# Performance work log

Hardware: AMD Instinct MI355X
Metric: run time of the kernel (lower is better)

Reference implementation:

```python
import jax, jax.numpy as jnp
import numpy as np

NUM_NODES = 100000
NUM_EDGES = 1600000
IN_DIM = 128
NUM_HEADS = 4
HEAD_DIM = 32  # out_dim=128, concat=True
NEG_SLOPE = 0.2
EPS = 1e-16


def setup_inputs() -> dict:
    key = jax.random.key(0)
    k1, k2, k3, k4 = jax.random.split(key, 4)
    node_features = jax.random.normal(k1, (NUM_NODES, IN_DIM), dtype=jnp.float32)
    edge_index = jax.random.randint(k2, (2, NUM_EDGES), 0, NUM_NODES, dtype=jnp.int64)
    W = jax.random.normal(k3, (IN_DIM, NUM_HEADS * HEAD_DIM), dtype=jnp.float32) * 0.05
    a = jax.random.normal(k4, (NUM_HEADS, 2 * HEAD_DIM), dtype=jnp.float32)
    return {"node_features": node_features, "edge_index": edge_index, "W": W, "a": a}


def reference(node_features, edge_index, W, a):
    N = node_features.shape[0]
    # h: [N, H, hd]
    h = (node_features @ W).reshape(N, NUM_HEADS, HEAD_DIM)
    src, dst = edge_index[0], edge_index[1]
    h_src = h[src]  # [E, H, hd]
    h_dst = h[dst]  # [E, H, hd]
    # a . cat(h_src, h_dst) split into two dots to avoid materializing h_cat
    scores = (jnp.einsum('ehd,hd->eh', h_src, a[:, :HEAD_DIM])
              + jnp.einsum('ehd,hd->eh', h_dst, a[:, HEAD_DIM:]))
    scores = jnp.where(scores >= 0, scores, NEG_SLOPE * scores)  # leaky_relu(0.2)
    # scatter-softmax over incoming edges of each dst node (unstabilized exp, as in source)
    exp_s = jnp.exp(scores)  # [E, H]
    sum_exp = jax.ops.segment_sum(exp_s, dst, num_segments=N)  # [N, H]
    attn = exp_s / (sum_exp[dst] + EPS)  # [E, H]
    # dropout is identity in eval mode
    weighted = h_src * attn[:, :, None]  # [E, H, hd]
    out = jax.ops.segment_sum(weighted.reshape(-1, NUM_HEADS * HEAD_DIM), dst, num_segments=N)
    return out  # [N, out_dim]
```

## Files before the change

kernel.cpp:

```cpp
#include <hip/hip_runtime.h>

#define NN 100000
#define NE 1600000

#define NRANGE 256
#define RDST 391
#define CAP 6800
#define EPB_A 16384
#define NCHA ((NE + EPB_A - 1) / EPB_A)
#define GEMM_BLK 1563

typedef __attribute__((ext_vector_type(8))) __bf16 bf16x8;
typedef __attribute__((ext_vector_type(4))) float  f32x4;

static __device__ __forceinline__ unsigned f2bf(float f) {
    unsigned u = __float_as_uint(f);
    return (u + 0x7fffu + ((u >> 16) & 1u)) >> 16;
}
static __device__ __forceinline__ float bf2f(unsigned b) {
    return __uint_as_float(b << 16);
}

union PkA { unsigned u[4]; bf16x8 b; };

__global__ __launch_bounds__(256) void kA_prep_bin(
    const float* __restrict__ W, const float* __restrict__ a,
    uint4* __restrict__ B0g, uint4* __restrict__ B1g,
    const int* __restrict__ ei, int* __restrict__ rangeRes,
    unsigned* __restrict__ bins)
{
    __shared__ float sWa[1024];
    __shared__ int cnt[NRANGE], base[NRANGE], cur[NRANGE];
    const int t = threadIdx.x;

    if (blockIdx.x == 0) {
        for (int e = t; e < 1024; e += 256) {
            int k = e >> 3, j = e & 7, q = j >> 1, s = j & 1;
            float sum = 0.f;
            #pragma unroll
            for (int c = 0; c < 32; ++c)
                sum = fmaf(W[k * 128 + q * 32 + c], a[q * 64 + s * 32 + c], sum);
            sWa[e] = sum;
        }
        __syncthreads();
        #pragma unroll
        for (int it = 0; it < 9; ++it) {
            int f  = it * 256 + t;
            int l  = f & 63;
            int tk = (f >> 6) & 3;
            int tn = f >> 8;
            int col = tn * 16 + (l & 15);
            int kk  = tk * 32 + ((l >> 4) << 3);
            unsigned hb[8], lb[8];
            #pragma unroll
            for (int j = 0; j < 8; ++j) {
                float w;
                if (col < 128)       w = W[(kk + j) * 128 + col];
                else if (col < 136)  w = sWa[(kk + j) * 8 + (col - 128)];
                else                 w = 0.f;
                hb[j] = f2bf(w);
                lb[j] = f2bf(w - bf2f(hb[j]));
            }
            B0g[f] = make_uint4(hb[0] | (hb[1] << 16), hb[2] | (hb[3] << 16),
                                hb[4] | (hb[5] << 16), hb[6] | (hb[7] << 16));
            B1g[f] = make_uint4(lb[0] | (lb[1] << 16), lb[2] | (lb[3] << 16),
                                lb[4] | (lb[5] << 16), lb[6] | (lb[7] << 16));
        }
        return;
    }

    const int c  = blockIdx.x - 1;
    const int b0 = c * EPB_A;
    const int b1 = min(NE, b0 + EPB_A);

    cnt[t] = 0;
    __syncthreads();
    for (int i = b0 + t; i < b1; i += 256)
        atomicAdd(&cnt[ei[NE + i] / RDST], 1);
    __syncthreads();
    base[t] = atomicAdd(&rangeRes[t * 16], cnt[t]) + t * CAP;
    cur[t] = 0;
    __syncthreads();
    for (int i = b0 + t; i < b1; i += 256) {
        int s = ei[i], d = ei[NE + i];
        int r = d / RDST;
        unsigned dloc = (unsigned)(d - r * RDST);
        int off = atomicAdd(&cur[r], 1);
        bins[base[r] + off] = (dloc << 17) | (unsigned)s;
    }
}

__global__ __launch_bounds__(256) void kB_gemm_build(
    const float* __restrict__ X, const uint4* __restrict__ B0g,
    const uint4* __restrict__ B1g, unsigned short* __restrict__ h16,
    float* __restrict__ asrc, float* __restrict__ adst,
    const int* __restrict__ rangeRes, const unsigned* __restrict__ bins,
    int* __restrict__ csr_src, int* __restrict__ cursor)
{
    __shared__ unsigned short B0[9 * 4 * 64 * 8];
    __shared__ unsigned short B1[9 * 4 * 64 * 8];
    const int tid = threadIdx.x;

    if (blockIdx.x < GEMM_BLK) {
        {
            uint4* s0 = (uint4*)B0;
            uint4* s1 = (uint4*)B1;
            #pragma unroll
            for (int it = 0; it < 9; ++it) {
                s0[it * 256 + tid] = B0g[it * 256 + tid];
                s1[it * 256 + tid] = B1g[it * 256 + tid];
            }
        }
        __syncthreads();

        const int w = tid >> 6;
        const int l = tid & 63;
        const int rowbase = blockIdx.x * 64 + w * 16;
        const int row = rowbase + (l & 15);
        const int rowc = row < NN ? row : (NN - 1);
        const float* xr = X + (size_t)rowc * 128 + ((l >> 4) << 3);

        f32x4 acc[9];
        #pragma unroll
        for (int t = 0; t < 9; ++t) acc[t] = (f32x4){0.f, 0.f, 0.f, 0.f};

        #pragma unroll
        for (int tk = 0; tk < 4; ++tk) {
            float4 xa = *(const float4*)(xr + tk * 32);
            float4 xb = *(const float4*)(xr + tk * 32 + 4);
            PkA pa;
            pa.u[0] = f2bf(xa.x) | (f2bf(xa.y) << 16);
            pa.u[1] = f2bf(xa.z) | (f2bf(xa.w) << 16);
            pa.u[2] = f2bf(xb.x) | (f2bf(xb.y) << 16);
            pa.u[3] = f2bf(xb.z) | (f2bf(xb.w) << 16);
            #pragma unroll
            for (int tn = 0; tn < 9; ++tn) {
                int off = (((tn << 2) + tk) * 64 + l) * 8;
                bf16x8 bh = *reinterpret_cast<const bf16x8*>(&B0[off]);
                bf16x8 bl = *reinterpret_cast<const bf16x8*>(&B1[off]);
                acc[tn] = __builtin_amdgcn_mfma_f32_16x16x32_bf16(pa.b, bh, acc[tn], 0, 0, 0);
                acc[tn] = __builtin_amdgcn_mfma_f32_16x16x32_bf16(pa.b, bl, acc[tn], 0, 0, 0);
            }
        }

        __syncthreads();

        const int g = l >> 4;
        unsigned short* hs = B0 + w * 2048;
        #pragma unroll
        for (int tn = 0; tn < 8; ++tn) {
            #pragma unroll
            for (int r = 0; r < 4; ++r)
                hs[((g << 2) + r) * 128 + (tn << 4) + (l & 15)] =
                    (unsigned short)f2bf(acc[tn][r]);
        }
        if ((l & 15) < 8) {
            int j = l & 15, q = j >> 1, s = j & 1;
            float* dp = s ? adst : asrc;
            #pragma unroll
            for (int r = 0; r < 4; ++r) {
                int rr = rowbase + (g << 2) + r;
                if (rr < NN) dp[rr * 4 + q] = acc[8][r];
            }
        }
        __syncthreads();

        if (rowbase < NN) {
            const uint4* sp = (const uint4*)hs;
            uint4* dp = (uint4*)(h16 + (size_t)rowbase * 128);
            #pragma unroll
            for (int i = 0; i < 4; ++i) dp[i * 64 + l] = sp[i * 64 + l];
        }
        return;
    }

    int* lenS = (int*)B0;
    int* hist = lenS + NRANGE;
    int* cur  = hist + 512;
    const int r = blockIdx.x - GEMM_BLK;
    const int t = tid;

    lenS[t] = rangeRes[t * 16];
    __syncthreads();
    for (int off = 1; off < NRANGE; off <<= 1) {
        int v = (t >= off) ? lenS[t - off] : 0;
        __syncthreads();
        lenS[t] += v;
        __syncthreads();
    }
    const int rangeOff = r ? lenS[r - 1] : 0;
    const int n = lenS[r] - rangeOff;
    const int lo = r * RDST;
    const int nd = min(RDST, NN - lo);

    hist[t] = 0; hist[t + 256] = 0;
    __syncthreads();
    const unsigned* bp = bins + (size_t)r * CAP;
    for (int i = t; i < n; i += 256)
        atomicAdd(&hist[bp[i] >> 17], 1);
    __syncthreads();
    for (int off = 1; off < 512; off <<= 1) {
        int i0 = t, i1 = t + 256;
        int v0 = (i0 >= off) ? hist[i0 - off] : 0;
        int v1 = (i1 >= off) ? hist[i1 - off] : 0;
        __syncthreads();
        hist[i0] += v0; hist[i1] += v1;
        __syncthreads();
    }
    for (int b = t; b < RDST; b += 256) cur[b] = b ? hist[b - 1] : 0;
    __syncthreads();
    for (int i = t; i < n; i += 256) {
        unsigned v = bp[i];
        int pos = atomicAdd(&cur[v >> 17], 1);
        csr_src[rangeOff + pos] = (int)(v & 0x1FFFFu);
    }
    __syncthreads();
    for (int b = t; b < nd; b += 256) cursor[lo + b] = rangeOff + cur[b];
}

__global__ __launch_bounds__(256) void k4_agg(
    const int* __restrict__ cursor, const int* __restrict__ csr_src,
    const float* __restrict__ asrc, const float* __restrict__ adst,
    const unsigned short* __restrict__ h16, float* __restrict__ out)
{
    int wid = (blockIdx.x * 256 + threadIdx.x) >> 6;
    if (wid >= NN) return;
    int l = threadIdx.x & 63;
    int g = l >> 4;
    int cidx = l & 15;
    int head = cidx >> 2;

    int end = cursor[wid];
    int beg = wid ? cursor[wid - 1] : 0;

    float ad = adst[(size_t)wid * 4 + head];

    float acc[8];
    #pragma unroll
    for (int c = 0; c < 8; ++c) acc[c] = 0.f;
    float sum = 0.f;

    int i = beg + g;
    if (i < end) {
        const int last = end - 1;
        int s0 = csr_src[i];
        int s1 = csr_src[min(i + 4,  last)];
        int s2 = csr_src[min(i + 8,  last)];
        int s3 = csr_src[min(i + 12, last)];
        do {
            int i2 = i + 16;
            int t0 = csr_src[min(i2,      last)];
            int t1 = csr_src[min(i2 + 4,  last)];
            int t2 = csr_src[min(i2 + 8,  last)];
            int t3 = csr_src[min(i2 + 12, last)];

            float a0 = asrc[(size_t)s0 * 4 + head];
            uint4 h0 = *(const uint4*)(h16 + (size_t)s0 * 128 + cidx * 8);
            float a1 = asrc[(size_t)s1 * 4 + head];
            uint4 h1 = *(const uint4*)(h16 + (size_t)s1 * 128 + cidx * 8);
            float a2 = asrc[(size_t)s2 * 4 + head];
            uint4 h2 = *(const uint4*)(h16 + (size_t)s2 * 128 + cidx * 8);
            float a3 = asrc[(size_t)s3 * 4 + head];
            uint4 h3 = *(const uint4*)(h16 + (size_t)s3 * 128 + cidx * 8);

            float sc0 = a0 + ad; sc0 = sc0 >= 0.f ? sc0 : 0.2f * sc0;
            float sc1 = a1 + ad; sc1 = sc1 >= 0.f ? sc1 : 0.2f * sc1;
            float sc2 = a2 + ad; sc2 = sc2 >= 0.f ? sc2 : 0.2f * sc2;
            float sc3 = a3 + ad; sc3 = sc3 >= 0.f ? sc3 : 0.2f * sc3;
            float w0 = __expf(sc0);
            float w1 = (i + 4  <= last) ? __expf(sc1) : 0.f;
            float w2 = (i + 8  <= last) ? __expf(sc2) : 0.f;
            float w3 = (i + 12 <= last) ? __expf(sc3) : 0.f;
            sum += (w0 + w1) + (w2 + w3);

            acc[0] = fmaf(w0, __uint_as_float(h0.x << 16),         acc[0]);
            acc[1] = fmaf(w0, __uint_as_float(h0.x & 0xffff0000u), acc[1]);
            acc[2] = fmaf(w0, __uint_as_float(h0.y << 16),         acc[2]);
            acc[3] = fmaf(w0, __uint_as_float(h0.y & 0xffff0000u), acc[3]);
            acc[4] = fmaf(w0, __uint_as_float(h0.z << 16),         acc[4]);
            acc[5] = fmaf(w0, __uint_as_float(h0.z & 0xffff0000u), acc[5]);
            acc[6] = fmaf(w0, __uint_as_float(h0.w << 16),         acc[6]);
            acc[7] = fmaf(w0, __uint_as_float(h0.w & 0xffff0000u), acc[7]);

            acc[0] = fmaf(w1, __uint_as_float(h1.x << 16),         acc[0]);
            acc[1] = fmaf(w1, __uint_as_float(h1.x & 0xffff0000u), acc[1]);
            acc[2] = fmaf(w1, __uint_as_float(h1.y << 16),         acc[2]);
            acc[3] = fmaf(w1, __uint_as_float(h1.y & 0xffff0000u), acc[3]);
            acc[4] = fmaf(w1, __uint_as_float(h1.z << 16),         acc[4]);
            acc[5] = fmaf(w1, __uint_as_float(h1.z & 0xffff0000u), acc[5]);
            acc[6] = fmaf(w1, __uint_as_float(h1.w << 16),         acc[6]);
            acc[7] = fmaf(w1, __uint_as_float(h1.w & 0xffff0000u), acc[7]);

            acc[0] = fmaf(w2, __uint_as_float(h2.x << 16),         acc[0]);
            acc[1] = fmaf(w2, __uint_as_float(h2.x & 0xffff0000u), acc[1]);
            acc[2] = fmaf(w2, __uint_as_float(h2.y << 16),         acc[2]);
            acc[3] = fmaf(w2, __uint_as_float(h2.y & 0xffff0000u), acc[3]);
            acc[4] = fmaf(w2, __uint_as_float(h2.z << 16),         acc[4]);
            acc[5] = fmaf(w2, __uint_as_float(h2.z & 0xffff0000u), acc[5]);
            acc[6] = fmaf(w2, __uint_as_float(h2.w << 16),         acc[6]);
            acc[7] = fmaf(w2, __uint_as_float(h2.w & 0xffff0000u), acc[7]);

            acc[0] = fmaf(w3, __uint_as_float(h3.x << 16),         acc[0]);
            acc[1] = fmaf(w3, __uint_as_float(h3.x & 0xffff0000u), acc[1]);
            acc[2] = fmaf(w3, __uint_as_float(h3.y << 16),         acc[2]);
            acc[3] = fmaf(w3, __uint_as_float(h3.y & 0xffff0000u), acc[3]);
            acc[4] = fmaf(w3, __uint_as_float(h3.z << 16),         acc[4]);
            acc[5] = fmaf(w3, __uint_as_float(h3.z & 0xffff0000u), acc[5]);
            acc[6] = fmaf(w3, __uint_as_float(h3.w << 16),         acc[6]);
            acc[7] = fmaf(w3, __uint_as_float(h3.w & 0xffff0000u), acc[7]);

            s0 = t0; s1 = t1; s2 = t2; s3 = t3; i = i2;
        } while (i < end);
    }

    #pragma unroll
    for (int c = 0; c < 8; ++c) {
        acc[c] += __shfl_xor(acc[c], 16);
        acc[c] += __shfl_xor(acc[c], 32);
    }
    sum += __shfl_xor(sum, 16);
    sum += __shfl_xor(sum, 32);

    if (g == 0) {
        float rs = 1.0f / (sum + 1e-16f);
        f32x4* ob = (f32x4*)(out + (size_t)wid * 128 + cidx * 8);
        f32x4 v0 = {acc[0] * rs, acc[1] * rs, acc[2] * rs, acc[3] * rs};
        f32x4 v1 = {acc[4] * rs, acc[5] * rs, acc[6] * rs, acc[7] * rs};
        __builtin_nontemporal_store(v0, ob);
        __builtin_nontemporal_store(v1, ob + 1);
    }
}

extern "C" void kernel_launch(void* const* d_in, const int* in_sizes, int n_in,
                              void* d_out, int out_size, void* d_ws, size_t ws_size,
                              hipStream_t stream)
{
    const float* X  = (const float*)d_in[0];
    const int*   ei = (const int*)d_in[1];
    const float* W  = (const float*)d_in[2];
    const float* a  = (const float*)d_in[3];
    float* out = (float*)d_out;

    unsigned short* h16 = (unsigned short*)d_ws;
    float* asrc     = (float*)d_ws + 6400000;
    float* adst     = asrc + 400000;
    int*   csr_src  = (int*)(adst + 400000);
    int*   cursor   = csr_src + 1600000;
    int*   rangeRes = cursor + 100000;
    uint4* B0g      = (uint4*)(rangeRes + NRANGE * 16);
    uint4* B1g      = B0g + 2304;
    unsigned* bins  = (unsigned*)(B1g + 2304);

    hipMemsetAsync(rangeRes, 0, NRANGE * 16 * sizeof(int), stream);

    kA_prep_bin<<<1 + NCHA, 256, 0, stream>>>(W, a, B0g, B1g, ei, rangeRes, bins);
    kB_gemm_build<<<GEMM_BLK + NRANGE, 256, 0, stream>>>(X, B0g, B1g, h16,
                                                         asrc, adst, rangeRes,
                                                         bins, csr_src, cursor);
    k4_agg<<<(NN * 64 + 255) / 256, 256, 0, stream>>>(cursor, csr_src,
                                                      asrc, adst, h16, out);
}
```

Measured before the change: 165.6 us.

## Process two 64-row tiles per GEMM block and shrink edge-binning chunk size

Each GEMM block now computes 128 rows by holding two sets of accumulators, so each B fragment read from LDS is reused across two row tiles and the B staging cost is spread over twice the rows. The GEMM grid is halved to match. The edge-binning chunk size also drops from 16384 to 4096 edges, giving more chunks and finer parallelism in that phase. In exchange the GEMM uses more accumulator registers (about 72 more VGPRs), which can lower occupancy, and the epilogue adds an extra barrier per tile.

```diff
diff --git a/kernel.cpp b/kernel.cpp
--- a/kernel.cpp
+++ b/kernel.cpp
@@ -6,9 +6,9 @@
 #define NRANGE 256
 #define RDST 391
 #define CAP 6800
-#define EPB_A 16384
+#define EPB_A 4096
 #define NCHA ((NE + EPB_A - 1) / EPB_A)
-#define GEMM_BLK 1563
+#define GEMM_BLK 782
 
 typedef __attribute__((ext_vector_type(8))) __bf16 bf16x8;
 typedef __attribute__((ext_vector_type(4))) float  f32x4;
@@ -115,31 +115,40 @@
 
         const int w = tid >> 6;
         const int l = tid & 63;
-        const int rowbase = blockIdx.x * 64 + w * 16;
-        const int row = rowbase + (l & 15);
-        const int rowc = row < NN ? row : (NN - 1);
-        const float* xr = X + (size_t)rowc * 128 + ((l >> 4) << 3);
-
-        f32x4 acc[9];
+        const int r0 = blockIdx.x * 128 + w * 16 + (l & 15);
+        const float* xr0 = X + (size_t)min(r0,      NN - 1) * 128 + ((l >> 4) << 3);
+        const float* xr1 = X + (size_t)min(r0 + 64, NN - 1) * 128 + ((l >> 4) << 3);
+
+        f32x4 acc[2][9];
         #pragma unroll
-        for (int t = 0; t < 9; ++t) acc[t] = (f32x4){0.f, 0.f, 0.f, 0.f};
+        for (int m = 0; m < 2; ++m)
+            #pragma unroll
+            for (int t = 0; t < 9; ++t) acc[m][t] = (f32x4){0.f, 0.f, 0.f, 0.f};
 
         #pragma unroll
         for (int tk = 0; tk < 4; ++tk) {
-            float4 xa = *(const float4*)(xr + tk * 32);
-            float4 xb = *(const float4*)(xr + tk * 32 + 4);
-            PkA pa;
-            pa.u[0] = f2bf(xa.x) | (f2bf(xa.y) << 16);
-            pa.u[1] = f2bf(xa.z) | (f2bf(xa.w) << 16);
-            pa.u[2] = f2bf(xb.x) | (f2bf(xb.y) << 16);
-            pa.u[3] = f2bf(xb.z) | (f2bf(xb.w) << 16);
+            float4 xa0 = *(const float4*)(xr0 + tk * 32);
+            float4 xb0 = *(const float4*)(xr0 + tk * 32 + 4);
+            float4 xa1 = *(const float4*)(xr1 + tk * 32);
+            float4 xb1 = *(const float4*)(xr1 + tk * 32 + 4);
+            PkA p0, p1;
+            p0.u[0] = f2bf(xa0.x) | (f2bf(xa0.y) << 16);
+            p0.u[1] = f2bf(xa0.z) | (f2bf(xa0.w) << 16);
+            p0.u[2] = f2bf(xb0.x) | (f2bf(xb0.y) << 16);
+            p0.u[3] = f2bf(xb0.z) | (f2bf(xb0.w) << 16);
+            p1.u[0] = f2bf(xa1.x) | (f2bf(xa1.y) << 16);
+            p1.u[1] = f2bf(xa1.z) | (f2bf(xa1.w) << 16);
+            p1.u[2] = f2bf(xb1.x) | (f2bf(xb1.y) << 16);
+            p1.u[3] = f2bf(xb1.z) | (f2bf(xb1.w) << 16);
             #pragma unroll
             for (int tn = 0; tn < 9; ++tn) {
                 int off = (((tn << 2) + tk) * 64 + l) * 8;
                 bf16x8 bh = *reinterpret_cast<const bf16x8*>(&B0[off]);
                 bf16x8 bl = *reinterpret_cast<const bf16x8*>(&B1[off]);
-                acc[tn] = __builtin_amdgcn_mfma_f32_16x16x32_bf16(pa.b, bh, acc[tn], 0, 0, 0);
-                acc[tn] = __builtin_amdgcn_mfma_f32_16x16x32_bf16(pa.b, bl, acc[tn], 0, 0, 0);
+                acc[0][tn] = __builtin_amdgcn_mfma_f32_16x16x32_bf16(p0.b, bh, acc[0][tn], 0, 0, 0);
+                acc[0][tn] = __builtin_amdgcn_mfma_f32_16x16x32_bf16(p0.b, bl, acc[0][tn], 0, 0, 0);
+                acc[1][tn] = __builtin_amdgcn_mfma_f32_16x16x32_bf16(p1.b, bh, acc[1][tn], 0, 0, 0);
+                acc[1][tn] = __builtin_amdgcn_mfma_f32_16x16x32_bf16(p1.b, bl, acc[1][tn], 0, 0, 0);
             }
         }
 
@@ -148,28 +157,32 @@
         const int g = l >> 4;
         unsigned short* hs = B0 + w * 2048;
         #pragma unroll
-        for (int tn = 0; tn < 8; ++tn) {
-            #pragma unroll
-            for (int r = 0; r < 4; ++r)
-                hs[((g << 2) + r) * 128 + (tn << 4) + (l & 15)] =
-                    (unsigned short)f2bf(acc[tn][r]);
-        }
-        if ((l & 15) < 8) {
-            int j = l & 15, q = j >> 1, s = j & 1;
-            float* dp = s ? adst : asrc;
-            #pragma unroll
-            for (int r = 0; r < 4; ++r) {
-                int rr = rowbase + (g << 2) + r;
-                if (rr < NN) dp[rr * 4 + q] = acc[8][r];
-            }
-        }
-        __syncthreads();
-
-        if (rowbase < NN) {
-            const uint4* sp = (const uint4*)hs;
-            uint4* dp = (uint4*)(h16 + (size_t)rowbase * 128);
-            #pragma unroll
-            for (int i = 0; i < 4; ++i) dp[i * 64 + l] = sp[i * 64 + l];
+        for (int mt = 0; mt < 2; ++mt) {
+            const int rowbase = blockIdx.x * 128 + mt * 64 + w * 16;
+            #pragma unroll
+            for (int tn = 0; tn < 8; ++tn) {
+                #pragma unroll
+                for (int r = 0; r < 4; ++r)
+                    hs[((g << 2) + r) * 128 + (tn << 4) + (l & 15)] =
+                        (unsigned short)f2bf(acc[mt][tn][r]);
+            }
+            if ((l & 15) < 8) {
+                int j = l & 15, q = j >> 1, s = j & 1;
+                float* dp = s ? adst : asrc;
+                #pragma unroll
+                for (int r = 0; r < 4; ++r) {
+                    int rr = rowbase + (g << 2) + r;
+                    if (rr < NN) dp[rr * 4 + q] = acc[mt][8][r];
+                }
+            }
+            __syncthreads();
+            if (rowbase < NN) {
+                const uint4* sp = (const uint4*)hs;
+                uint4* dp = (uint4*)(h16 + (size_t)rowbase * 128);
+                #pragma unroll
+                for (int i = 0; i < 4; ++i) dp[i * 64 + l] = sp[i * 64 + l];
+            }
+            __syncthreads();
         }
         return;
     }
```

Result: faster. 138.4 us (-16.4%).
